# Kernel optimization log

Hardware: AMD Instinct MI355X
Metric: run time of the kernel (lower is better)

## Reference

```python
import jax, jax.numpy as jnp
import numpy as np

N, C, H, E = 4096, 512, 8, 131072
D = C // H
ALPHA = 0.5
EPS = 1e-5


def layer_norm(x, g, b):
    mu = jnp.mean(x, axis=-1, keepdims=True)
    var = jnp.mean((x - mu) ** 2, axis=-1, keepdims=True)
    return (x - mu) * jax.lax.rsqrt(var + EPS) * g + b


def setup_inputs() -> dict:
    key = jax.random.key(0)
    ks = jax.random.split(key, 20)
    s = 0.02
    return {
        "x": jax.random.normal(ks[0], (N, C), jnp.float32),
        "edge_index": jax.random.randint(ks[1], (2, E), 0, N, jnp.int32),
        "local_w": jax.random.normal(ks[2], (C, C), jnp.float32) * s,
        "local_b": jnp.zeros((C,), jnp.float32),
        "in_proj_w": jax.random.normal(ks[3], (3 * C, C), jnp.float32) * s,
        "in_proj_b": jnp.zeros((3 * C,), jnp.float32),
        "attn_out_w": jax.random.normal(ks[4], (C, C), jnp.float32) * s,
        "attn_out_b": jnp.zeros((C,), jnp.float32),
        "output_w": jax.random.normal(ks[5], (C, C), jnp.float32) * s,
        "output_b": jnp.zeros((C,), jnp.float32),
        "norm1_g": jnp.ones((C,), jnp.float32),
        "norm1_b": jnp.zeros((C,), jnp.float32),
        "norm2_g": jnp.ones((C,), jnp.float32),
        "norm2_b": jnp.zeros((C,), jnp.float32),
        "ffn_w1": jax.random.normal(ks[6], (2 * C, C), jnp.float32) * s,
        "ffn_b1": jnp.zeros((2 * C,), jnp.float32),
        "ffn_w2": jax.random.normal(ks[7], (C, 2 * C), jnp.float32) * s,
        "ffn_b2": jnp.zeros((C,), jnp.float32),
    }


def reference(x, edge_index, local_w, local_b, in_proj_w, in_proj_b,
              attn_out_w, attn_out_b, output_w, output_b,
              norm1_g, norm1_b, norm2_g, norm2_b,
              ffn_w1, ffn_b1, ffn_w2, ffn_b2):
    src, dst = edge_index[0], edge_index[1]

    # local branch: linear then scatter-mean over incoming edges
    local_h = x @ local_w.T + local_b                       # [N,C]
    summed = jax.ops.segment_sum(local_h[src], dst, num_segments=N)
    cnt = jax.ops.segment_sum(jnp.ones((E,), x.dtype), dst, num_segments=N)
    local_out = summed / jnp.maximum(cnt, 1.0)[:, None]

    # global branch: full self-attention over all nodes
    qkv = x @ in_proj_w.T + in_proj_b                       # [N,3C]
    q, k, v = jnp.split(qkv, 3, axis=-1)
    q = q.reshape(N, H, D)
    k = k.reshape(N, H, D)
    v = v.reshape(N, H, D)
    scores = jnp.einsum('nhd,mhd->hnm', q, k) / jnp.sqrt(jnp.asarray(D, x.dtype))
    attn = jax.nn.softmax(scores, axis=-1)                  # [H,N,N]
    ctx = jnp.einsum('hnm,mhd->nhd', attn, v).reshape(N, C)
    global_out = ctx @ attn_out_w.T + attn_out_b

    mixed = ALPHA * local_out + (1.0 - ALPHA) * global_out
    hidden = layer_norm(x + (mixed @ output_w.T + output_b), norm1_g, norm1_b)

    ff = jax.nn.gelu(hidden @ ffn_w1.T + ffn_b1, approximate=False) @ ffn_w2.T + ffn_b2
    return layer_norm(hidden + ff, norm2_g, norm2_b)
```

## Files before the change

### kernel.cpp

```cpp
#include <hip/hip_runtime.h>


#define N_NODES 4096
#define C_DIM   512
#define H_HEADS 8
#define D_HEAD  64
#define E_EDGES 131072

typedef unsigned short u16;
typedef unsigned int   u32;
typedef u16   u16x8  __attribute__((ext_vector_type(8)));
typedef __bf16 bf16x8 __attribute__((ext_vector_type(8)));
typedef float  f32x4  __attribute__((ext_vector_type(4)));

__device__ __forceinline__ float b2f(u16 u) {
  unsigned int i = ((unsigned int)u) << 16;
  return __builtin_bit_cast(float, i);
}
__device__ __forceinline__ u16 f2b(float f) {
  unsigned int i = __builtin_bit_cast(unsigned int, f);
  i += 0x7fffu + ((i >> 16) & 1u);
  return (u16)(i >> 16);
}
__device__ __forceinline__ u16 f2b_up(float f) {
  unsigned int i = __builtin_bit_cast(unsigned int, f);
  return (u16)((i + 0x8000u) >> 16);
}
__device__ __forceinline__ void glds16(const u16* g, u16* l) {
  __builtin_amdgcn_global_load_lds(
      (const __attribute__((address_space(1))) void*)g,
      (__attribute__((address_space(3))) void*)l, 16, 0, 0);
}

struct CvtArgs {
  const float* src[7];
  u16* dst[7];
  int n[7];
  const int* ei;
  int* deg;
};

__global__ __launch_bounds__(256) void cvt_multi(CvtArgs a) {
  const int t = blockIdx.y;
  if (t == 7) {
    if (blockIdx.x >= E_EDGES / 256) return;
    const int e = blockIdx.x * 256 + threadIdx.x;
    atomicAdd(&a.deg[a.ei[E_EDGES + e]], 1);
    return;
  }
  const int i = (blockIdx.x * 256 + threadIdx.x) * 8;
  if (i >= a.n[t]) return;
  const float* s = a.src[t] + i;
  f32x4 v0 = *(const f32x4*)s;
  f32x4 v1 = *(const f32x4*)(s + 4);
  u16x8 o;
  o[0]=f2b(v0[0]); o[1]=f2b(v0[1]); o[2]=f2b(v0[2]); o[3]=f2b(v0[3]);
  o[4]=f2b(v1[0]); o[5]=f2b(v1[1]); o[6]=f2b(v1[2]); o[7]=f2b(v1[3]);
  *(u16x8*)(a.dst[t] + i) = o;
}

template<int EPI>
__global__ __launch_bounds__(256) void gemm_bt(
    const u16* __restrict__ A, const u16* __restrict__ W,
    const float* __restrict__ bias, void* __restrict__ outp,
    int M, int Nout, int K,
    const float* __restrict__ mloc)
{
  const int tid  = threadIdx.x;
  const int lane = tid & 63, wave = tid >> 6;
  const int quad = lane >> 4, l16 = lane & 15;
  const int wm = wave >> 1, wn = wave & 1;
  const int bm = blockIdx.x, bnb = blockIdx.y;

  __shared__ __align__(16) u16 As[64][64];
  __shared__ __align__(16) u16 Ws[64][64];

  f32x4 acc[2][2] = {};

  const int lr = lane >> 3, gs = lane & 7;
  const int g8 = (gs ^ lr) * 8;
  const u16* a0 = A + (size_t)(bm  * 64 + wave * 16 +     lr) * K + g8;
  const u16* a1 = A + (size_t)(bm  * 64 + wave * 16 + 8 + lr) * K + g8;
  const u16* w0 = W + (size_t)(bnb * 64 + wave * 16 +     lr) * K + g8;
  const u16* w1 = W + (size_t)(bnb * 64 + wave * 16 + 8 + lr) * K + g8;

  for (int k0 = 0; k0 < K; k0 += 64) {
    __syncthreads();
    glds16(a0 + k0, &As[wave * 16][0]);
    glds16(a1 + k0, &As[wave * 16 + 8][0]);
    glds16(w0 + k0, &Ws[wave * 16][0]);
    glds16(w1 + k0, &Ws[wave * 16 + 8][0]);
    __syncthreads();
#pragma unroll
    for (int ks = 0; ks < 2; ++ks) {
      const int slot = ((ks * 4 + quad) ^ (l16 & 7)) * 8;
      bf16x8 af[2], bf[2];
      af[0] = *(const bf16x8*)&As[wm * 32 +      l16][slot];
      af[1] = *(const bf16x8*)&As[wm * 32 + 16 + l16][slot];
      bf[0] = *(const bf16x8*)&Ws[wn * 32 +      l16][slot];
      bf[1] = *(const bf16x8*)&Ws[wn * 32 + 16 + l16][slot];
#pragma unroll
      for (int i = 0; i < 2; ++i)
#pragma unroll
        for (int j = 0; j < 2; ++j)
          acc[i][j] = __builtin_amdgcn_mfma_f32_16x16x32_bf16(af[i], bf[j], acc[i][j], 0, 0, 0);
    }
  }

#pragma unroll
  for (int i = 0; i < 2; ++i)
#pragma unroll
    for (int j = 0; j < 2; ++j) {
      const int col = bnb * 64 + wn * 32 + j * 16 + l16;
      const float bias_v = bias[col];
#pragma unroll
      for (int r = 0; r < 4; ++r) {
        const int row = bm * 64 + wm * 32 + i * 16 + quad * 4 + r;
        float v = acc[i][j][r] + bias_v;
        const size_t o = (size_t)row * Nout + col;
        if constexpr (EPI == 1) {
          ((float*)outp)[o] = v;
        } else {
          ((u16*)outp)[o] = f2b(0.5f * mloc[o] + 0.5f * v);
        }
      }
    }
}

template<int MODE>
__global__ __launch_bounds__(256) void gemm128(
    const u16* __restrict__ A, const u16* __restrict__ W,
    const float* __restrict__ bias0, const float* __restrict__ bias1,
    u16* __restrict__ out0, u16* __restrict__ out1,
    int M, int Nout, int K)
{
  const int tid  = threadIdx.x;
  const int lane = tid & 63, wave = tid >> 6;
  const int quad = lane >> 4, l16 = lane & 15;
  const int wm = wave >> 1, wn = wave & 1;
  const int bm = blockIdx.x, bnb = blockIdx.y;

  __shared__ __align__(16) u16 As[128][64];
  __shared__ __align__(16) u16 Ws[128][64];

  f32x4 acc[4][4] = {};

  const int lr = lane >> 3, gs = lane & 7;
  const int g8 = (gs ^ lr) * 8;
  const u16* ab = A + (size_t)(bm  * 128 + wave * 32 + lr) * K + g8;
  const u16* wb = W + (size_t)(bnb * 128 + wave * 32 + lr) * K + g8;

  for (int k0 = 0; k0 < K; k0 += 64) {
    __syncthreads();
#pragma unroll
    for (int c = 0; c < 4; ++c) {
      glds16(ab + (size_t)(c * 8) * K + k0, &As[wave * 32 + c * 8][0]);
      glds16(wb + (size_t)(c * 8) * K + k0, &Ws[wave * 32 + c * 8][0]);
    }
    __syncthreads();
#pragma unroll
    for (int ks = 0; ks < 2; ++ks) {
      const int slot = ((ks * 4 + quad) ^ (l16 & 7)) * 8;
      bf16x8 af[4], bf[4];
#pragma unroll
      for (int am = 0; am < 4; ++am)
        af[am] = *(const bf16x8*)&As[wm * 64 + am * 16 + l16][slot];
#pragma unroll
      for (int bn = 0; bn < 4; ++bn)
        bf[bn] = *(const bf16x8*)&Ws[wn * 64 + bn * 16 + l16][slot];
#pragma unroll
      for (int am = 0; am < 4; ++am)
#pragma unroll
        for (int bn = 0; bn < 4; ++bn)
          acc[am][bn] = __builtin_amdgcn_mfma_f32_16x16x32_bf16(af[am], bf[bn], acc[am][bn], 0, 0, 0);
    }
  }

#pragma unroll
  for (int am = 0; am < 4; ++am)
#pragma unroll
    for (int bn = 0; bn < 4; ++bn) {
      const int col = bnb * 128 + wn * 64 + bn * 16 + l16;
      float bias_v;
      if constexpr (MODE == 0) bias_v = (col < 512) ? bias0[col] : bias1[col - 512];
      else                     bias_v = bias0[col];
#pragma unroll
      for (int r = 0; r < 4; ++r) {
        const int row = bm * 128 + wm * 64 + am * 16 + quad * 4 + r;
        float v = acc[am][bn][r] + bias_v;
        if constexpr (MODE == 0) {
          if (col < 512) out0[(size_t)row * 512 + col] = f2b(v);
          else           out1[(size_t)row * 1536 + (col - 512)] = f2b(v);
        } else {
          float gl = 0.5f * v * (1.0f + erff(v * 0.70710678118654752f));
          out0[(size_t)row * Nout + col] = f2b(gl);
        }
      }
    }
}

__global__ __launch_bounds__(256) void scan_kernel(
    const int* __restrict__ deg, int* __restrict__ off, int* __restrict__ cursor)
{
  __shared__ int part[256];
  const int t = threadIdx.x;
  int v[16];
  int s = 0;
#pragma unroll
  for (int i = 0; i < 16; ++i) { v[i] = deg[t * 16 + i]; s += v[i]; }
  part[t] = s;
  __syncthreads();
  for (int d = 1; d < 256; d <<= 1) {
    int val = (t >= d) ? part[t - d] : 0;
    __syncthreads();
    if (t >= d) part[t] += val;
    __syncthreads();
  }
  int prefix = (t == 0) ? 0 : part[t - 1];
#pragma unroll
  for (int i = 0; i < 16; ++i) {
    off[t * 16 + i] = prefix;
    cursor[t * 16 + i] = prefix;
    prefix += v[i];
  }
  if (t == 255) off[4096] = prefix;
}

__global__ __launch_bounds__(256) void fill_kernel(
    const int* __restrict__ ei, int* __restrict__ cursor, int* __restrict__ csr)
{
  const int e = blockIdx.x * 256 + threadIdx.x;
  const int s = ei[e];
  const int d = ei[E_EDGES + e];
  const int p = atomicAdd(&cursor[d], 1);
  csr[p] = s;
}

__global__ __launch_bounds__(256) void gather_kernel(
    const int* __restrict__ off, const int* __restrict__ csr,
    const u16* __restrict__ lh, float* __restrict__ lo)
{
  const int wave = threadIdx.x >> 6, lane = threadIdx.x & 63;
  const int n = blockIdx.x * 4 + wave;
  const int j0 = off[n], j1 = off[n + 1];
  float acc[8] = {};
  for (int j = j0; j < j1; ++j) {
    const int s = csr[j];
    const u16x8 v = *(const u16x8*)(lh + (size_t)s * C_DIM + lane * 8);
#pragma unroll
    for (int i = 0; i < 8; ++i) acc[i] += b2f(v[i]);
  }
  const float inv = 1.0f / fmaxf((float)(j1 - j0), 1.0f);
  f32x4 o0, o1;
#pragma unroll
  for (int i = 0; i < 4; ++i) { o0[i] = acc[i] * inv; o1[i] = acc[4 + i] * inv; }
  float* op = lo + (size_t)n * C_DIM + lane * 8;
  *(f32x4*)op = o0;
  *(f32x4*)(op + 4) = o1;
}

__global__ __launch_bounds__(256) void vtrans_kernel(
    const u16* __restrict__ qkv, u16* __restrict__ vt)
{
  const int tid = threadIdx.x;
  const int d = tid & 63, mg = tid >> 6;
  const int h = blockIdx.y, mt = blockIdx.x;
  const int m0 = mt * 64 + mg * 16;
  u16 buf[16];
#pragma unroll
  for (int i = 0; i < 16; ++i)
    buf[i] = qkv[(size_t)(m0 + i) * 1536 + 1024 + h * 64 + d];
  u16x8 w0, w1;
#pragma unroll
  for (int i = 0; i < 8; ++i) { w0[i] = buf[i]; w1[i] = buf[8 + i]; }
  u16* op = vt + (size_t)(h * 64 + d) * N_NODES + m0;
  *(u16x8*)op = w0;
  *(u16x8*)(op + 8) = w1;
}

template<int SPLITS>
__global__ __launch_bounds__(256) void attn_kernel(
    const u16* __restrict__ qkv, const u16* __restrict__ vt,
    float* __restrict__ opart, float* __restrict__ lpart)
{
  const int tid = threadIdx.x, wave = tid >> 6, lane = tid & 63;
  const int quad = lane >> 4, l16 = lane & 15;
  const int h = blockIdx.y, tile = blockIdx.x, split = blockIdx.z;

  __shared__ __align__(16) u16 Ks[64][64];
  __shared__ __align__(16) u16 Vts[64][64];
  __shared__ __align__(16) u16 Ps[128][72];

  const float QSCALE = 0.18033688011112042f;
  bf16x8 aq[2][2];
#pragma unroll
  for (int mb = 0; mb < 2; ++mb) {
    const int qrow = tile * 128 + wave * 32 + mb * 16 + l16;
    const u16* qp = qkv + (size_t)qrow * 1536 + h * 64 + quad * 8;
    u16x8 q0 = *(const u16x8*)qp;
    u16x8 q1 = *(const u16x8*)(qp + 32);
    u16x8 s0, s1;
#pragma unroll
    for (int i = 0; i < 8; ++i) {
      s0[i] = f2b(b2f(q0[i]) * QSCALE);
      s1[i] = f2b(b2f(q1[i]) * QSCALE);
    }
    aq[mb][0] = __builtin_bit_cast(bf16x8, s0);
    aq[mb][1] = __builtin_bit_cast(bf16x8, s1);
  }

  f32x4 O[2][4] = {};
  float lsum[2][4] = {};

  const int lr = lane >> 3, gs = lane & 7;
  const int g8 = (gs ^ lr) * 8;
  const int R0 = wave * 16 + lr;

  const int mt1 = (split + 1) * (64 / SPLITS);
  for (int mt = split * (64 / SPLITS); mt < mt1; ++mt) {
    __syncthreads();
    glds16(qkv + (size_t)(mt * 64 + R0)     * 1536 + 512 + h * 64 + g8, &Ks[wave * 16][0]);
    glds16(qkv + (size_t)(mt * 64 + R0 + 8) * 1536 + 512 + h * 64 + g8, &Ks[wave * 16 + 8][0]);
    glds16(vt + (size_t)(h * 64 + R0)     * N_NODES + mt * 64 + g8, &Vts[wave * 16][0]);
    glds16(vt + (size_t)(h * 64 + R0 + 8) * N_NODES + mt * 64 + g8, &Vts[wave * 16 + 8][0]);
    __syncthreads();

    f32x4 s[2][4] = {};
#pragma unroll
    for (int ks = 0; ks < 2; ++ks) {
      const int slot = ((ks * 4 + quad) ^ (l16 & 7)) * 8;
      bf16x8 bk[4];
#pragma unroll
      for (int jn = 0; jn < 4; ++jn)
        bk[jn] = *(const bf16x8*)&Ks[jn * 16 + l16][slot];
#pragma unroll
      for (int mb = 0; mb < 2; ++mb)
#pragma unroll
        for (int jn = 0; jn < 4; ++jn)
          s[mb][jn] = __builtin_amdgcn_mfma_f32_16x16x32_bf16(aq[mb][ks], bk[jn], s[mb][jn], 0, 0, 0);
    }

#pragma unroll
    for (int mb = 0; mb < 2; ++mb)
#pragma unroll
      for (int jn = 0; jn < 4; ++jn)
#pragma unroll
        for (int r = 0; r < 4; ++r) {
          float p = __builtin_amdgcn_exp2f(s[mb][jn][r]);
          lsum[mb][r] += p;
          Ps[wave * 32 + mb * 16 + quad * 4 + r][jn * 16 + l16] = f2b_up(p);
        }

#pragma unroll
    for (int ks = 0; ks < 2; ++ks) {
      const int slot = ((ks * 4 + quad) ^ (l16 & 7)) * 8;
      bf16x8 bv[4];
#pragma unroll
      for (int jd = 0; jd < 4; ++jd)
        bv[jd] = *(const bf16x8*)&Vts[jd * 16 + l16][slot];
#pragma unroll
      for (int mb = 0; mb < 2; ++mb) {
        bf16x8 ap = *(const bf16x8*)&Ps[wave * 32 + mb * 16 + l16][ks * 32 + quad * 8];
#pragma unroll
        for (int jd = 0; jd < 4; ++jd)
          O[mb][jd] = __builtin_amdgcn_mfma_f32_16x16x32_bf16(ap, bv[jd], O[mb][jd], 0, 0, 0);
      }
    }
  }

#pragma unroll
  for (int mb = 0; mb < 2; ++mb)
#pragma unroll
    for (int r = 0; r < 4; ++r)
#pragma unroll
      for (int off = 1; off < 16; off <<= 1)
        lsum[mb][r] += __shfl_xor(lsum[mb][r], off);

#pragma unroll
  for (int mb = 0; mb < 2; ++mb)
#pragma unroll
    for (int r = 0; r < 4; ++r) {
      const int row = tile * 128 + wave * 32 + mb * 16 + quad * 4 + r;
      float* orow = opart + ((size_t)split * N_NODES + row) * C_DIM + h * 64;
#pragma unroll
      for (int jd = 0; jd < 4; ++jd)
        orow[jd * 16 + l16] = O[mb][jd][r];
      if (l16 == 0)
        lpart[((size_t)split * N_NODES + row) * H_HEADS + h] = lsum[mb][r];
    }
}

template<int SPLITS>
__global__ __launch_bounds__(256) void attn_combine(
    const float* __restrict__ opart, const float* __restrict__ lpart,
    u16* __restrict__ ctx)
{
  const size_t base = (size_t)(blockIdx.x * 256 + threadIdx.x) * 8;
  const int row = (int)(base >> 9);
  const int h = (int)((base & 511) >> 6);
  float l = 0.0f;
#pragma unroll
  for (int s = 0; s < SPLITS; ++s)
    l += lpart[(size_t)s * N_NODES * H_HEADS + (size_t)row * H_HEADS + h];
  const float inv = 1.0f / l;
  float o[8] = {};
#pragma unroll
  for (int s = 0; s < SPLITS; ++s) {
    const float* op = opart + (size_t)s * N_NODES * C_DIM + base;
    f32x4 p0 = *(const f32x4*)op;
    f32x4 p1 = *(const f32x4*)(op + 4);
#pragma unroll
    for (int i = 0; i < 4; ++i) { o[i] += p0[i]; o[4 + i] += p1[i]; }
  }
  u16x8 ob;
#pragma unroll
  for (int i = 0; i < 8; ++i) ob[i] = f2b(o[i] * inv);
  *(u16x8*)(ctx + base) = ob;
}

__global__ __launch_bounds__(256) void ln1_kernel(
    const float* __restrict__ x, const float* __restrict__ pr,
    const float* __restrict__ g, const float* __restrict__ b,
    u16* __restrict__ hb, float* __restrict__ hf)
{
  const int wave = threadIdx.x >> 6, lane = threadIdx.x & 63;
  const int row = blockIdx.x * 4 + wave;
  const int c0 = lane * 8;
  const size_t base = (size_t)row * C_DIM + c0;
  f32x4 x0 = *(const f32x4*)(x + base);
  f32x4 x1 = *(const f32x4*)(x + base + 4);
  f32x4 p0 = *(const f32x4*)(pr + base);
  f32x4 p1 = *(const f32x4*)(pr + base + 4);
  float v[8];
#pragma unroll
  for (int i = 0; i < 4; ++i) { v[i] = x0[i] + p0[i]; v[4 + i] = x1[i] + p1[i]; }
  float sum = 0, sq = 0;
#pragma unroll
  for (int i = 0; i < 8; ++i) { sum += v[i]; sq += v[i] * v[i]; }
  for (int off = 1; off < 64; off <<= 1) { sum += __shfl_xor(sum, off); sq += __shfl_xor(sq, off); }
  const float mean = sum * (1.0f / C_DIM);
  const float var  = sq * (1.0f / C_DIM) - mean * mean;
  const float rstd = rsqrtf(var + 1e-5f);
  f32x4 g0 = *(const f32x4*)(g + c0), g1 = *(const f32x4*)(g + c0 + 4);
  f32x4 b0 = *(const f32x4*)(b + c0), b1 = *(const f32x4*)(b + c0 + 4);
  u16x8 ob; f32x4 h0, h1;
#pragma unroll
  for (int i = 0; i < 4; ++i) {
    float hv0 = (v[i]     - mean) * rstd * g0[i] + b0[i];
    float hv1 = (v[4 + i] - mean) * rstd * g1[i] + b1[i];
    h0[i] = hv0; h1[i] = hv1;
    ob[i] = f2b(hv0); ob[4 + i] = f2b(hv1);
  }
  *(u16x8*)(hb + base) = ob;
  *(f32x4*)(hf + base) = h0;
  *(f32x4*)(hf + base + 4) = h1;
}

__global__ __launch_bounds__(256) void ln2_kernel(
    const float* __restrict__ a, const float* __restrict__ c,
    const float* __restrict__ g, const float* __restrict__ b,
    float* __restrict__ out)
{
  const int wave = threadIdx.x >> 6, lane = threadIdx.x & 63;
  const int row = blockIdx.x * 4 + wave;
  const int c0 = lane * 8;
  const size_t base = (size_t)row * C_DIM + c0;
  f32x4 a0 = *(const f32x4*)(a + base), a1 = *(const f32x4*)(a + base + 4);
  f32x4 c0v = *(const f32x4*)(c + base), c1v = *(const f32x4*)(c + base + 4);
  float v[8];
#pragma unroll
  for (int i = 0; i < 4; ++i) { v[i] = a0[i] + c0v[i]; v[4 + i] = a1[i] + c1v[i]; }
  float sum = 0, sq = 0;
#pragma unroll
  for (int i = 0; i < 8; ++i) { sum += v[i]; sq += v[i] * v[i]; }
  for (int off = 1; off < 64; off <<= 1) { sum += __shfl_xor(sum, off); sq += __shfl_xor(sq, off); }
  const float mean = sum * (1.0f / C_DIM);
  const float var  = sq * (1.0f / C_DIM) - mean * mean;
  const float rstd = rsqrtf(var + 1e-5f);
  f32x4 g0 = *(const f32x4*)(g + c0), g1 = *(const f32x4*)(g + c0 + 4);
  f32x4 b0 = *(const f32x4*)(b + c0), b1 = *(const f32x4*)(b + c0 + 4);
  f32x4 h0, h1;
#pragma unroll
  for (int i = 0; i < 4; ++i) {
    h0[i] = (v[i]     - mean) * rstd * g0[i] + b0[i];
    h1[i] = (v[4 + i] - mean) * rstd * g1[i] + b1[i];
  }
  *(f32x4*)(out + base) = h0;
  *(f32x4*)(out + base + 4) = h1;
}

extern "C" void kernel_launch(void* const* d_in, const int* in_sizes, int n_in,
                              void* d_out, int out_size, void* d_ws, size_t ws_size,
                              hipStream_t stream) {
  const float* x          = (const float*)d_in[0];
  const int*   ei         = (const int*)d_in[1];
  const float* local_w    = (const float*)d_in[2];
  const float* local_b    = (const float*)d_in[3];
  const float* in_proj_w  = (const float*)d_in[4];
  const float* in_proj_b  = (const float*)d_in[5];
  const float* attn_out_w = (const float*)d_in[6];
  const float* attn_out_b = (const float*)d_in[7];
  const float* output_w   = (const float*)d_in[8];
  const float* output_b   = (const float*)d_in[9];
  const float* n1g = (const float*)d_in[10];
  const float* n1b = (const float*)d_in[11];
  const float* n2g = (const float*)d_in[12];
  const float* n2b = (const float*)d_in[13];
  const float* ffn_w1 = (const float*)d_in[14];
  const float* ffn_b1 = (const float*)d_in[15];
  const float* ffn_w2 = (const float*)d_in[16];
  const float* ffn_b2 = (const float*)d_in[17];
  float* out = (float*)d_out;

  char* ws = (char*)d_ws;
  size_t o = 0;
  float* local_out = (float*)(ws + o); o += (size_t)N_NODES * C_DIM * 4;
  int* deg    = (int*)(ws + o); o += (N_NODES) * 4;
  int* off    = (int*)(ws + o); o += (N_NODES + 16) * 4;
  int* cursor = (int*)(ws + o); o += (N_NODES) * 4;
  int* csr    = (int*)(ws + o); o += (size_t)E_EDGES * 4;
  u16* xb   = (u16*)(ws + o); o += (size_t)N_NODES * C_DIM * 2;
  u16* wbLQ = (u16*)(ws + o); o += (size_t)4 * C_DIM * C_DIM * 2;
  u16* wbA  = (u16*)(ws + o); o += (size_t)C_DIM * C_DIM * 2;
  u16* wbO  = (u16*)(ws + o); o += (size_t)C_DIM * C_DIM * 2;
  u16* wbF1 = (u16*)(ws + o); o += (size_t)2 * C_DIM * C_DIM * 2;
  u16* wbF2 = (u16*)(ws + o); o += (size_t)2 * C_DIM * C_DIM * 2;
  u16* local_h   = (u16*)(ws + o); o += (size_t)N_NODES * C_DIM * 2;
  u16* qkvb      = (u16*)(ws + o); o += (size_t)N_NODES * 3 * C_DIM * 2;
  u16* ctxb      = (u16*)(ws + o); o += (size_t)N_NODES * C_DIM * 2;
  u16* mixed     = (u16*)(ws + o); o += (size_t)N_NODES * C_DIM * 2;
  u16* hidden_bf = (u16*)(ws + o); o += (size_t)N_NODES * C_DIM * 2;
  float* hidden_f = (float*)(ws + o); o += (size_t)N_NODES * C_DIM * 4;
  u16* ff1       = (u16*)(ws + o); o += (size_t)N_NODES * 2 * C_DIM * 2;
  float* proj  = (float*)qkvb;
  float* ff2   = (float*)local_out;
  u16*   vt    = xb;
  float* opart4 = (float*)(ws + o);
  float* lpart4 = (float*)(ws + o + (size_t)4 * N_NODES * C_DIM * 4);
  const size_t need4 = o + (size_t)4 * N_NODES * C_DIM * 4 + (size_t)4 * N_NODES * H_HEADS * 4;
  const bool use4 = (ws_size >= need4);
  float* opart2 = (float*)hidden_bf;
  float* lpart2 = opart2 + (size_t)2 * N_NODES * C_DIM;

  (void)hipMemsetAsync(deg, 0, N_NODES * 4, stream);

  CvtArgs ca;
  ca.src[0] = x;          ca.dst[0] = xb;   ca.n[0] = N_NODES * C_DIM;
  ca.src[1] = local_w;    ca.dst[1] = wbLQ;                  ca.n[1] = C_DIM * C_DIM;
  ca.src[2] = in_proj_w;  ca.dst[2] = wbLQ + C_DIM * C_DIM;  ca.n[2] = 3 * C_DIM * C_DIM;
  ca.src[3] = attn_out_w; ca.dst[3] = wbA;  ca.n[3] = C_DIM * C_DIM;
  ca.src[4] = output_w;   ca.dst[4] = wbO;  ca.n[4] = C_DIM * C_DIM;
  ca.src[5] = ffn_w1;     ca.dst[5] = wbF1; ca.n[5] = 2 * C_DIM * C_DIM;
  ca.src[6] = ffn_w2;     ca.dst[6] = wbF2; ca.n[6] = 2 * C_DIM * C_DIM;
  ca.ei = ei; ca.deg = deg;
  cvt_multi<<<dim3(N_NODES * C_DIM / 2048, 8), 256, 0, stream>>>(ca);

  scan_kernel<<<1, 256, 0, stream>>>(deg, off, cursor);
  fill_kernel<<<E_EDGES / 256, 256, 0, stream>>>(ei, cursor, csr);

  gemm128<0><<<dim3(32, 16), 256, 0, stream>>>(xb, wbLQ, local_b, in_proj_b,
      local_h, qkvb, N_NODES, 4 * C_DIM, C_DIM);
  gather_kernel<<<N_NODES / 4, 256, 0, stream>>>(off, csr, local_h, local_out);

  vtrans_kernel<<<dim3(64, 8), 256, 0, stream>>>(qkvb, vt);
  if (use4) {
    attn_kernel<4><<<dim3(32, 8, 4), 256, 0, stream>>>(qkvb, vt, opart4, lpart4);
    attn_combine<4><<<N_NODES * C_DIM / 2048, 256, 0, stream>>>(opart4, lpart4, ctxb);
  } else {
    attn_kernel<2><<<dim3(32, 8, 2), 256, 0, stream>>>(qkvb, vt, opart2, lpart2);
    attn_combine<2><<<N_NODES * C_DIM / 2048, 256, 0, stream>>>(opart2, lpart2, ctxb);
  }

  gemm_bt<3><<<dim3(64, 8), 256, 0, stream>>>(ctxb, wbA, attn_out_b, mixed,
      N_NODES, C_DIM, C_DIM, local_out);

  gemm_bt<1><<<dim3(64, 8), 256, 0, stream>>>(mixed, wbO, output_b, proj,
      N_NODES, C_DIM, C_DIM, nullptr);
  ln1_kernel<<<N_NODES / 4, 256, 0, stream>>>(x, proj, n1g, n1b, hidden_bf, hidden_f);

  gemm128<2><<<dim3(32, 8), 256, 0, stream>>>(hidden_bf, wbF1, ffn_b1, nullptr,
      ff1, nullptr, N_NODES, 2 * C_DIM, C_DIM);
  gemm_bt<1><<<dim3(64, 8), 256, 0, stream>>>(ff1, wbF2, ffn_b2, ff2,
      N_NODES, C_DIM, 2 * C_DIM, nullptr);
  ln2_kernel<<<N_NODES / 4, 256, 0, stream>>>(hidden_f, ff2, n2g, n2b, out);
}
```

Measured before the change: 290.3 us.

## Fold attention-output projection into output projection via precomputed concatenated weight

```diff
diff --git a/kernel.cpp b/kernel.cpp
--- a/kernel.cpp
+++ b/kernel.cpp
@@ -38,6 +38,12 @@
   int n[7];
   const int* ei;
   int* deg;
+  u16* wbAT;
+  u16* wcat0;
+  const float* wo_f32;
+  const float* ba_f32;
+  const float* bo_f32;
+  float* bprime;
 };
 
 __global__ __launch_bounds__(256) void cvt_multi(CvtArgs a) {
@@ -46,6 +52,19 @@
     if (blockIdx.x >= E_EDGES / 256) return;
     const int e = blockIdx.x * 256 + threadIdx.x;
     atomicAdd(&a.deg[a.ei[E_EDGES + e]], 1);
+    return;
+  }
+  if (t == 8) {
+    const int n = blockIdx.x * 256 + threadIdx.x;
+    if (n >= 512) return;
+    const float* wrow = a.wo_f32 + (size_t)n * 512;
+    float s = 0.0f;
+    for (int k = 0; k < 512; k += 4) {
+      f32x4 w4 = *(const f32x4*)(wrow + k);
+      f32x4 b4 = *(const f32x4*)(a.ba_f32 + k);
+      s += w4[0] * b4[0] + w4[1] * b4[1] + w4[2] * b4[2] + w4[3] * b4[3];
+    }
+    a.bprime[n] = a.bo_f32[n] + 0.5f * s;
     return;
   }
   const int i = (blockIdx.x * 256 + threadIdx.x) * 8;
@@ -56,15 +75,27 @@
   u16x8 o;
   o[0]=f2b(v0[0]); o[1]=f2b(v0[1]); o[2]=f2b(v0[2]); o[3]=f2b(v0[3]);
   o[4]=f2b(v1[0]); o[5]=f2b(v1[1]); o[6]=f2b(v1[2]); o[7]=f2b(v1[3]);
+  if (t == 3) {
+    const int r = i >> 9, c = i & 511;
+#pragma unroll
+    for (int j = 0; j < 8; ++j) a.wbAT[(size_t)(c + j) * 512 + r] = o[j];
+    return;
+  }
   *(u16x8*)(a.dst[t] + i) = o;
+  if (t == 4) {
+    const int r = i >> 9, c = i & 511;
+    u16x8 oh;
+    oh[0]=f2b(v0[0]*0.5f); oh[1]=f2b(v0[1]*0.5f); oh[2]=f2b(v0[2]*0.5f); oh[3]=f2b(v0[3]*0.5f);
+    oh[4]=f2b(v1[0]*0.5f); oh[5]=f2b(v1[1]*0.5f); oh[6]=f2b(v1[2]*0.5f); oh[7]=f2b(v1[3]*0.5f);
+    *(u16x8*)(a.wcat0 + (size_t)r * 1024 + c) = oh;
+  }
 }
 
 template<int EPI>
 __global__ __launch_bounds__(256) void gemm_bt(
     const u16* __restrict__ A, const u16* __restrict__ W,
     const float* __restrict__ bias, void* __restrict__ outp,
-    int M, int Nout, int K,
-    const float* __restrict__ mloc)
+    int M, int Nout, int K)
 {
   const int tid  = threadIdx.x;
   const int lane = tid & 63, wave = tid >> 6;
@@ -112,7 +143,7 @@
 #pragma unroll
     for (int j = 0; j < 2; ++j) {
       const int col = bnb * 64 + wn * 32 + j * 16 + l16;
-      const float bias_v = bias[col];
+      const float bias_v = (EPI == 1) ? bias[col] : 0.0f;
 #pragma unroll
       for (int r = 0; r < 4; ++r) {
         const int row = bm * 64 + wm * 32 + i * 16 + quad * 4 + r;
@@ -121,7 +152,7 @@
         if constexpr (EPI == 1) {
           ((float*)outp)[o] = v;
         } else {
-          ((u16*)outp)[o] = f2b(0.5f * mloc[o] + 0.5f * v);
+          ((u16*)outp)[o] = f2b(0.5f * v);
         }
       }
     }
@@ -236,46 +267,44 @@
   csr[p] = s;
 }
 
-__global__ __launch_bounds__(256) void gather_kernel(
+__global__ __launch_bounds__(256) void gather_vtrans(
     const int* __restrict__ off, const int* __restrict__ csr,
-    const u16* __restrict__ lh, float* __restrict__ lo)
-{
-  const int wave = threadIdx.x >> 6, lane = threadIdx.x & 63;
-  const int n = blockIdx.x * 4 + wave;
-  const int j0 = off[n], j1 = off[n + 1];
-  float acc[8] = {};
-  for (int j = j0; j < j1; ++j) {
-    const int s = csr[j];
-    const u16x8 v = *(const u16x8*)(lh + (size_t)s * C_DIM + lane * 8);
-#pragma unroll
-    for (int i = 0; i < 8; ++i) acc[i] += b2f(v[i]);
-  }
-  const float inv = 1.0f / fmaxf((float)(j1 - j0), 1.0f);
-  f32x4 o0, o1;
-#pragma unroll
-  for (int i = 0; i < 4; ++i) { o0[i] = acc[i] * inv; o1[i] = acc[4 + i] * inv; }
-  float* op = lo + (size_t)n * C_DIM + lane * 8;
-  *(f32x4*)op = o0;
-  *(f32x4*)(op + 4) = o1;
-}
-
-__global__ __launch_bounds__(256) void vtrans_kernel(
+    const u16* __restrict__ lh, u16* __restrict__ ast,
     const u16* __restrict__ qkv, u16* __restrict__ vt)
 {
-  const int tid = threadIdx.x;
-  const int d = tid & 63, mg = tid >> 6;
-  const int h = blockIdx.y, mt = blockIdx.x;
-  const int m0 = mt * 64 + mg * 16;
-  u16 buf[16];
-#pragma unroll
-  for (int i = 0; i < 16; ++i)
-    buf[i] = qkv[(size_t)(m0 + i) * 1536 + 1024 + h * 64 + d];
-  u16x8 w0, w1;
-#pragma unroll
-  for (int i = 0; i < 8; ++i) { w0[i] = buf[i]; w1[i] = buf[8 + i]; }
-  u16* op = vt + (size_t)(h * 64 + d) * N_NODES + m0;
-  *(u16x8*)op = w0;
-  *(u16x8*)(op + 8) = w1;
+  if (blockIdx.y == 0) {
+    const int wave = threadIdx.x >> 6, lane = threadIdx.x & 63;
+    const int n = blockIdx.x * 4 + wave;
+    const int j0 = off[n], j1 = off[n + 1];
+    float acc[8] = {};
+    for (int j = j0; j < j1; ++j) {
+      const int s = csr[j];
+      const u16x8 v = *(const u16x8*)(lh + (size_t)s * C_DIM + lane * 8);
+#pragma unroll
+      for (int i = 0; i < 8; ++i) acc[i] += b2f(v[i]);
+    }
+    const float inv = 1.0f / fmaxf((float)(j1 - j0), 1.0f);
+    u16x8 ob;
+#pragma unroll
+    for (int i = 0; i < 8; ++i) ob[i] = f2b(acc[i] * inv);
+    *(u16x8*)(ast + (size_t)n * 1024 + lane * 8) = ob;
+  } else {
+    if (blockIdx.x >= 512) return;
+    const int tid = threadIdx.x;
+    const int d = tid & 63, mg = tid >> 6;
+    const int h = blockIdx.x >> 6, mt = blockIdx.x & 63;
+    const int m0 = mt * 64 + mg * 16;
+    u16 buf[16];
+#pragma unroll
+    for (int i = 0; i < 16; ++i)
+      buf[i] = qkv[(size_t)(m0 + i) * 1536 + 1024 + h * 64 + d];
+    u16x8 w0, w1;
+#pragma unroll
+    for (int i = 0; i < 8; ++i) { w0[i] = buf[i]; w1[i] = buf[8 + i]; }
+    u16* op = vt + (size_t)(h * 64 + d) * N_NODES + m0;
+    *(u16x8*)op = w0;
+    *(u16x8*)(op + 8) = w1;
+  }
 }
 
 template<int SPLITS>
@@ -393,7 +422,7 @@
 template<int SPLITS>
 __global__ __launch_bounds__(256) void attn_combine(
     const float* __restrict__ opart, const float* __restrict__ lpart,
-    u16* __restrict__ ctx)
+    u16* __restrict__ ast)
 {
   const size_t base = (size_t)(blockIdx.x * 256 + threadIdx.x) * 8;
   const int row = (int)(base >> 9);
@@ -415,7 +444,7 @@
   u16x8 ob;
 #pragma unroll
   for (int i = 0; i < 8; ++i) ob[i] = f2b(o[i] * inv);
-  *(u16x8*)(ctx + base) = ob;
+  *(u16x8*)(ast + (size_t)row * 1024 + 512 + (base & 511)) = ob;
 }
 
 __global__ __launch_bounds__(256) void ln1_kernel(
@@ -514,27 +543,27 @@
 
   char* ws = (char*)d_ws;
   size_t o = 0;
-  float* local_out = (float*)(ws + o); o += (size_t)N_NODES * C_DIM * 4;
+  u16* ast = (u16*)(ws + o); o += (size_t)N_NODES * 1024 * 2;
   int* deg    = (int*)(ws + o); o += (N_NODES) * 4;
   int* off    = (int*)(ws + o); o += (N_NODES + 16) * 4;
   int* cursor = (int*)(ws + o); o += (N_NODES) * 4;
   int* csr    = (int*)(ws + o); o += (size_t)E_EDGES * 4;
   u16* xb   = (u16*)(ws + o); o += (size_t)N_NODES * C_DIM * 2;
   u16* wbLQ = (u16*)(ws + o); o += (size_t)4 * C_DIM * C_DIM * 2;
-  u16* wbA  = (u16*)(ws + o); o += (size_t)C_DIM * C_DIM * 2;
+  u16* wbAT = (u16*)(ws + o); o += (size_t)C_DIM * C_DIM * 2;
   u16* wbO  = (u16*)(ws + o); o += (size_t)C_DIM * C_DIM * 2;
+  u16* wcat = (u16*)(ws + o); o += (size_t)C_DIM * 1024 * 2;
   u16* wbF1 = (u16*)(ws + o); o += (size_t)2 * C_DIM * C_DIM * 2;
   u16* wbF2 = (u16*)(ws + o); o += (size_t)2 * C_DIM * C_DIM * 2;
+  float* bprime = (float*)(ws + o); o += 512 * 4;
   u16* local_h   = (u16*)(ws + o); o += (size_t)N_NODES * C_DIM * 2;
   u16* qkvb      = (u16*)(ws + o); o += (size_t)N_NODES * 3 * C_DIM * 2;
-  u16* ctxb      = (u16*)(ws + o); o += (size_t)N_NODES * C_DIM * 2;
-  u16* mixed     = (u16*)(ws + o); o += (size_t)N_NODES * C_DIM * 2;
   u16* hidden_bf = (u16*)(ws + o); o += (size_t)N_NODES * C_DIM * 2;
   float* hidden_f = (float*)(ws + o); o += (size_t)N_NODES * C_DIM * 4;
   u16* ff1       = (u16*)(ws + o); o += (size_t)N_NODES * 2 * C_DIM * 2;
-  float* proj  = (float*)qkvb;
-  float* ff2   = (float*)local_out;
-  u16*   vt    = xb;
+  float* proj = (float*)qkvb;
+  float* ff2  = (float*)ast;
+  u16*   vt   = xb;
   float* opart4 = (float*)(ws + o);
   float* lpart4 = (float*)(ws + o + (size_t)4 * N_NODES * C_DIM * 4);
   const size_t need4 = o + (size_t)4 * N_NODES * C_DIM * 4 + (size_t)4 * N_NODES * H_HEADS * 4;
@@ -548,39 +577,43 @@
   ca.src[0] = x;          ca.dst[0] = xb;   ca.n[0] = N_NODES * C_DIM;
   ca.src[1] = local_w;    ca.dst[1] = wbLQ;                  ca.n[1] = C_DIM * C_DIM;
   ca.src[2] = in_proj_w;  ca.dst[2] = wbLQ + C_DIM * C_DIM;  ca.n[2] = 3 * C_DIM * C_DIM;
-  ca.src[3] = attn_out_w; ca.dst[3] = wbA;  ca.n[3] = C_DIM * C_DIM;
+  ca.src[3] = attn_out_w; ca.dst[3] = nullptr;               ca.n[3] = C_DIM * C_DIM;
   ca.src[4] = output_w;   ca.dst[4] = wbO;  ca.n[4] = C_DIM * C_DIM;
   ca.src[5] = ffn_w1;     ca.dst[5] = wbF1; ca.n[5] = 2 * C_DIM * C_DIM;
   ca.src[6] = ffn_w2;     ca.dst[6] = wbF2; ca.n[6] = 2 * C_DIM * C_DIM;
   ca.ei = ei; ca.deg = deg;
-  cvt_multi<<<dim3(N_NODES * C_DIM / 2048, 8), 256, 0, stream>>>(ca);
+  ca.wbAT = wbAT; ca.wcat0 = wcat;
+  ca.wo_f32 = output_w; ca.ba_f32 = attn_out_b; ca.bo_f32 = output_b;
+  ca.bprime = bprime;
+  cvt_multi<<<dim3(N_NODES * C_DIM / 2048, 9), 256, 0, stream>>>(ca);
 
   scan_kernel<<<1, 256, 0, stream>>>(deg, off, cursor);
   fill_kernel<<<E_EDGES / 256, 256, 0, stream>>>(ei, cursor, csr);
 
+  gemm_bt<5><<<dim3(8, 8), 256, 0, stream>>>(wbO, wbAT, nullptr,
+      wcat + 512, 512, 1024, 512);
+
   gemm128<0><<<dim3(32, 16), 256, 0, stream>>>(xb, wbLQ, local_b, in_proj_b,
       local_h, qkvb, N_NODES, 4 * C_DIM, C_DIM);
-  gather_kernel<<<N_NODES / 4, 256, 0, stream>>>(off, csr, local_h, local_out);
-
-  vtrans_kernel<<<dim3(64, 8), 256, 0, stream>>>(qkvb, vt);
+
+  gather_vtrans<<<dim3(N_NODES / 4, 2), 256, 0, stream>>>(off, csr, local_h,
+      ast, qkvb, vt);
+
   if (use4) {
     attn_kernel<4><<<dim3(32, 8, 4), 256, 0, stream>>>(qkvb, vt, opart4, lpart4);
-    attn_combine<4><<<N_NODES * C_DIM / 2048, 256, 0, stream>>>(opart4, lpart4, ctxb);
+    attn_combine<4><<<N_NODES * C_DIM / 2048, 256, 0, stream>>>(opart4, lpart4, ast);
   } else {
     attn_kernel<2><<<dim3(32, 8, 2), 256, 0, stream>>>(qkvb, vt, opart2, lpart2);
-    attn_combine<2><<<N_NODES * C_DIM / 2048, 256, 0, stream>>>(opart2, lpart2, ctxb);
-  }
-
-  gemm_bt<3><<<dim3(64, 8), 256, 0, stream>>>(ctxb, wbA, attn_out_b, mixed,
-      N_NODES, C_DIM, C_DIM, local_out);
-
-  gemm_bt<1><<<dim3(64, 8), 256, 0, stream>>>(mixed, wbO, output_b, proj,
-      N_NODES, C_DIM, C_DIM, nullptr);
+    attn_combine<2><<<N_NODES * C_DIM / 2048, 256, 0, stream>>>(opart2, lpart2, ast);
+  }
+
+  gemm_bt<1><<<dim3(64, 8), 256, 0, stream>>>(ast, wcat, bprime, proj,
+      N_NODES, C_DIM, 1024);
   ln1_kernel<<<N_NODES / 4, 256, 0, stream>>>(x, proj, n1g, n1b, hidden_bf, hidden_f);
 
   gemm128<2><<<dim3(32, 8), 256, 0, stream>>>(hidden_bf, wbF1, ffn_b1, nullptr,
       ff1, nullptr, N_NODES, 2 * C_DIM, C_DIM);
   gemm_bt<1><<<dim3(64, 8), 256, 0, stream>>>(ff1, wbF2, ffn_b2, ff2,
-      N_NODES, C_DIM, 2 * C_DIM, nullptr);
+      N_NODES, C_DIM, 2 * C_DIM);
   ln2_kernel<<<N_NODES / 4, 256, 0, stream>>>(hidden_f, ff2, n2g, n2b, out);
 }
```

After: 301.5 us. +3.9%, slower.

## Merge gather and V-transpose launches, MFMA row sums, bf16 attention partials

Applied to the files above, without the earlier changes.

```diff
diff --git a/kernel.cpp b/kernel.cpp
--- a/kernel.cpp
+++ b/kernel.cpp
@@ -236,52 +236,52 @@
   csr[p] = s;
 }
 
-__global__ __launch_bounds__(256) void gather_kernel(
+__global__ __launch_bounds__(256) void gather_vtrans(
     const int* __restrict__ off, const int* __restrict__ csr,
-    const u16* __restrict__ lh, float* __restrict__ lo)
-{
-  const int wave = threadIdx.x >> 6, lane = threadIdx.x & 63;
-  const int n = blockIdx.x * 4 + wave;
-  const int j0 = off[n], j1 = off[n + 1];
-  float acc[8] = {};
-  for (int j = j0; j < j1; ++j) {
-    const int s = csr[j];
-    const u16x8 v = *(const u16x8*)(lh + (size_t)s * C_DIM + lane * 8);
-#pragma unroll
-    for (int i = 0; i < 8; ++i) acc[i] += b2f(v[i]);
-  }
-  const float inv = 1.0f / fmaxf((float)(j1 - j0), 1.0f);
-  f32x4 o0, o1;
-#pragma unroll
-  for (int i = 0; i < 4; ++i) { o0[i] = acc[i] * inv; o1[i] = acc[4 + i] * inv; }
-  float* op = lo + (size_t)n * C_DIM + lane * 8;
-  *(f32x4*)op = o0;
-  *(f32x4*)(op + 4) = o1;
-}
-
-__global__ __launch_bounds__(256) void vtrans_kernel(
+    const u16* __restrict__ lh, float* __restrict__ lo,
     const u16* __restrict__ qkv, u16* __restrict__ vt)
 {
-  const int tid = threadIdx.x;
-  const int d = tid & 63, mg = tid >> 6;
-  const int h = blockIdx.y, mt = blockIdx.x;
-  const int m0 = mt * 64 + mg * 16;
-  u16 buf[16];
-#pragma unroll
-  for (int i = 0; i < 16; ++i)
-    buf[i] = qkv[(size_t)(m0 + i) * 1536 + 1024 + h * 64 + d];
-  u16x8 w0, w1;
-#pragma unroll
-  for (int i = 0; i < 8; ++i) { w0[i] = buf[i]; w1[i] = buf[8 + i]; }
-  u16* op = vt + (size_t)(h * 64 + d) * N_NODES + m0;
-  *(u16x8*)op = w0;
-  *(u16x8*)(op + 8) = w1;
+  if (blockIdx.y == 0) {
+    const int wave = threadIdx.x >> 6, lane = threadIdx.x & 63;
+    const int n = blockIdx.x * 4 + wave;
+    const int j0 = off[n], j1 = off[n + 1];
+    float acc[8] = {};
+    for (int j = j0; j < j1; ++j) {
+      const int s = csr[j];
+      const u16x8 v = *(const u16x8*)(lh + (size_t)s * C_DIM + lane * 8);
+#pragma unroll
+      for (int i = 0; i < 8; ++i) acc[i] += b2f(v[i]);
+    }
+    const float inv = 1.0f / fmaxf((float)(j1 - j0), 1.0f);
+    f32x4 o0, o1;
+#pragma unroll
+    for (int i = 0; i < 4; ++i) { o0[i] = acc[i] * inv; o1[i] = acc[4 + i] * inv; }
+    float* op = lo + (size_t)n * C_DIM + lane * 8;
+    *(f32x4*)op = o0;
+    *(f32x4*)(op + 4) = o1;
+  } else {
+    if (blockIdx.x >= 512) return;
+    const int tid = threadIdx.x;
+    const int d = tid & 63, mg = tid >> 6;
+    const int h = blockIdx.x >> 6, mt = blockIdx.x & 63;
+    const int m0 = mt * 64 + mg * 16;
+    u16 buf[16];
+#pragma unroll
+    for (int i = 0; i < 16; ++i)
+      buf[i] = qkv[(size_t)(m0 + i) * 1536 + 1024 + h * 64 + d];
+    u16x8 w0, w1;
+#pragma unroll
+    for (int i = 0; i < 8; ++i) { w0[i] = buf[i]; w1[i] = buf[8 + i]; }
+    u16* op = vt + (size_t)(h * 64 + d) * N_NODES + m0;
+    *(u16x8*)op = w0;
+    *(u16x8*)(op + 8) = w1;
+  }
 }
 
 template<int SPLITS>
 __global__ __launch_bounds__(256) void attn_kernel(
     const u16* __restrict__ qkv, const u16* __restrict__ vt,
-    float* __restrict__ opart, float* __restrict__ lpart)
+    u16* __restrict__ opart, float* __restrict__ lpart)
 {
   const int tid = threadIdx.x, wave = tid >> 6, lane = tid & 63;
   const int quad = lane >> 4, l16 = lane & 15;
@@ -309,8 +309,13 @@
     aq[mb][1] = __builtin_bit_cast(bf16x8, s1);
   }
 
+  u16x8 ones_u;
+#pragma unroll
+  for (int i = 0; i < 8; ++i) ones_u[i] = 0x3F80;
+  const bf16x8 bones = __builtin_bit_cast(bf16x8, ones_u);
+
   f32x4 O[2][4] = {};
-  float lsum[2][4] = {};
+  f32x4 Lacc[2] = {};
 
   const int lr = lane >> 3, gs = lane & 7;
   const int g8 = (gs ^ lr) * 8;
@@ -347,7 +352,6 @@
 #pragma unroll
         for (int r = 0; r < 4; ++r) {
           float p = __builtin_amdgcn_exp2f(s[mb][jn][r]);
-          lsum[mb][r] += p;
           Ps[wave * 32 + mb * 16 + quad * 4 + r][jn * 16 + l16] = f2b_up(p);
         }
 
@@ -364,35 +368,28 @@
 #pragma unroll
         for (int jd = 0; jd < 4; ++jd)
           O[mb][jd] = __builtin_amdgcn_mfma_f32_16x16x32_bf16(ap, bv[jd], O[mb][jd], 0, 0, 0);
+        Lacc[mb] = __builtin_amdgcn_mfma_f32_16x16x32_bf16(ap, bones, Lacc[mb], 0, 0, 0);
       }
     }
   }
-
-#pragma unroll
-  for (int mb = 0; mb < 2; ++mb)
-#pragma unroll
-    for (int r = 0; r < 4; ++r)
-#pragma unroll
-      for (int off = 1; off < 16; off <<= 1)
-        lsum[mb][r] += __shfl_xor(lsum[mb][r], off);
 
 #pragma unroll
   for (int mb = 0; mb < 2; ++mb)
 #pragma unroll
     for (int r = 0; r < 4; ++r) {
       const int row = tile * 128 + wave * 32 + mb * 16 + quad * 4 + r;
-      float* orow = opart + ((size_t)split * N_NODES + row) * C_DIM + h * 64;
+      u16* orow = opart + ((size_t)split * N_NODES + row) * C_DIM + h * 64;
 #pragma unroll
       for (int jd = 0; jd < 4; ++jd)
-        orow[jd * 16 + l16] = O[mb][jd][r];
+        orow[jd * 16 + l16] = f2b(O[mb][jd][r]);
       if (l16 == 0)
-        lpart[((size_t)split * N_NODES + row) * H_HEADS + h] = lsum[mb][r];
+        lpart[((size_t)split * N_NODES + row) * H_HEADS + h] = Lacc[mb][r];
     }
 }
 
 template<int SPLITS>
 __global__ __launch_bounds__(256) void attn_combine(
-    const float* __restrict__ opart, const float* __restrict__ lpart,
+    const u16* __restrict__ opart, const float* __restrict__ lpart,
     u16* __restrict__ ctx)
 {
   const size_t base = (size_t)(blockIdx.x * 256 + threadIdx.x) * 8;
@@ -406,11 +403,9 @@
   float o[8] = {};
 #pragma unroll
   for (int s = 0; s < SPLITS; ++s) {
-    const float* op = opart + (size_t)s * N_NODES * C_DIM + base;
-    f32x4 p0 = *(const f32x4*)op;
-    f32x4 p1 = *(const f32x4*)(op + 4);
-#pragma unroll
-    for (int i = 0; i < 4; ++i) { o[i] += p0[i]; o[4 + i] += p1[i]; }
+    const u16x8 p = *(const u16x8*)(opart + (size_t)s * N_NODES * C_DIM + base);
+#pragma unroll
+    for (int i = 0; i < 8; ++i) o[i] += b2f(p[i]);
   }
   u16x8 ob;
 #pragma unroll
@@ -535,12 +530,12 @@
   float* proj  = (float*)qkvb;
   float* ff2   = (float*)local_out;
   u16*   vt    = xb;
-  float* opart4 = (float*)(ws + o);
-  float* lpart4 = (float*)(ws + o + (size_t)4 * N_NODES * C_DIM * 4);
-  const size_t need4 = o + (size_t)4 * N_NODES * C_DIM * 4 + (size_t)4 * N_NODES * H_HEADS * 4;
+  u16* opart4 = (u16*)(ws + o);
+  float* lpart4 = (float*)(ws + o + (size_t)4 * N_NODES * C_DIM * 2);
+  const size_t need4 = o + (size_t)4 * N_NODES * C_DIM * 2 + (size_t)4 * N_NODES * H_HEADS * 4;
   const bool use4 = (ws_size >= need4);
-  float* opart2 = (float*)hidden_bf;
-  float* lpart2 = opart2 + (size_t)2 * N_NODES * C_DIM;
+  u16* opart2 = (u16*)hidden_bf;
+  float* lpart2 = (float*)(opart2 + (size_t)2 * N_NODES * C_DIM);
 
   (void)hipMemsetAsync(deg, 0, N_NODES * 4, stream);
 
@@ -560,9 +555,10 @@
 
   gemm128<0><<<dim3(32, 16), 256, 0, stream>>>(xb, wbLQ, local_b, in_proj_b,
       local_h, qkvb, N_NODES, 4 * C_DIM, C_DIM);
-  gather_kernel<<<N_NODES / 4, 256, 0, stream>>>(off, csr, local_h, local_out);
-
-  vtrans_kernel<<<dim3(64, 8), 256, 0, stream>>>(qkvb, vt);
+
+  gather_vtrans<<<dim3(N_NODES / 4, 2), 256, 0, stream>>>(off, csr, local_h,
+      local_out, qkvb, vt);
+
   if (use4) {
     attn_kernel<4><<<dim3(32, 8, 4), 256, 0, stream>>>(qkvb, vt, opart4, lpart4);
     attn_combine<4><<<N_NODES * C_DIM / 2048, 256, 0, stream>>>(opart4, lpart4, ctxb);
```

Measured after the change: 295.3 us. Within noise of the previous version (+1.7%).
